# Optimization experiments

Hardware: AMD Instinct MI355X
Metric: run time of the kernel (lower is better)

Reference implementation:

```python
import jax, jax.numpy as jnp
import numpy as np

# ---- module hyperparameters (from init_kwargs) ----
KL_TEMP = 4.0
NUM_CLASSES = 100
POLICY_NUMS = 7          # linear out dim = POLICY_NUMS + 2 (identity, classes, policies)
FEATURE_NUMS = 128       # linear in dim = concat of two 64-d policy features
POS_W = (1.0, 0.5, 0.001)
NEG_W = (1.0, 0.5, 0.001)
KD_CE_W = (1.0, 1.0)
LOSS_W = (1.0, 1.0, 1.0)
BATCH = 2048


def setup_inputs() -> dict:
    key = jax.random.key(0)
    ks = jax.random.split(key, 9)
    O = POLICY_NUMS + 2
    return {
        "student_logits": jax.random.normal(ks[0], (BATCH, NUM_CLASSES), jnp.float32),
        "teacher_logits": jax.random.normal(ks[1], (BATCH, NUM_CLASSES), jnp.float32),
        "student_policy": jax.random.normal(ks[2], (BATCH, FEATURE_NUMS // 2), jnp.float32),
        "teacher_policy": jax.random.normal(ks[3], (BATCH, FEATURE_NUMS // 2), jnp.float32),
        "W1": jax.random.normal(ks[4], (O, FEATURE_NUMS), jnp.float32) * 0.08,  # frozen teacher linear
        "bias1": jax.random.normal(ks[5], (O,), jnp.float32) * 0.01,
        "W2": jax.random.normal(ks[6], (O, FEATURE_NUMS), jnp.float32) * 0.08,  # trainable student linear
        "bias2": jax.random.normal(ks[7], (O,), jnp.float32) * 0.01,
        "targets": jax.random.randint(ks[8], (BATCH, 1, POLICY_NUMS + 1), 0, 10, dtype=jnp.int32),
    }


def _kldiv_mean(inp, tgt):
    # torch KLDivLoss(reduction='mean'): mean over all elems of target*(log(target)-input), zero where target<=0
    safe = jnp.where(tgt > 0, tgt, 1.0)
    return jnp.where(tgt > 0, tgt * (jnp.log(safe) - inp), 0.0).mean()


def _wmean(loss, tgt, pw, nw):
    return jnp.where(tgt == 1.0, loss * pw, loss * nw).mean()


def _pair_linear(feat, W, bias):
    # L[i, j] = W @ concat(f_even[j], f_odd[i]) + bias, computed without materializing [b1,b1,2f]
    f = feat.shape[-1]
    f1, f2 = feat[0::2], feat[1::2]                       # [b1, f] each
    A = f1 @ W[:, :f].T                                   # [b1, O]  (j part)
    B = f2 @ W[:, f:].T                                   # [b1, O]  (i part)
    return B[:, None, :] + A[None, :, :] + bias           # [b1, b1, O]


def _policy_loss(teacher_policy, student_policy, targets, W1, bias1, W2, bias2):
    B = student_policy.shape[0]
    b1 = B // 2
    dt = student_policy.dtype

    Ls = _pair_linear(student_policy, W2, bias2)          # [b1,b1,O]
    Lt = jax.lax.stop_gradient(_pair_linear(teacher_policy, W1, bias1))

    sI, sC = Ls[..., 0], Ls[..., 1]
    sP = Ls[..., 2:].reshape(b1 * b1, POLICY_NUMS)
    tI, tC = Lt[..., 0], Lt[..., 1]
    tP = Lt[..., 2:].reshape(b1 * b1, POLICY_NUMS)

    eye = jnp.eye(b1, dtype=dt)
    # off-diagonal identity entries are detached for the student (teacher already no-grad)
    sI = eye * sI + (1.0 - eye) * jax.lax.stop_gradient(sI)

    t = targets.reshape(B, POLICY_NUMS + 1)
    t1, t2 = t[0::2], t[1::2]
    Teq = (t1[None, :, :] == t2[:, None, :]).astype(dt)   # [b1,b1,P+1]

    classes_value = 1.0 / (NUM_CLASSES - 1) + 1.0
    identity_value = 1.0 / (b1 - 1) + 1.0
    gC = Teq[..., 0] * classes_value - 1.0 / (NUM_CLASSES - 1)
    gP = Teq[..., 1:].reshape(b1 * b1, POLICY_NUMS) * 2.0 - 1.0
    gI = eye * identity_value - 1.0 / (b1 - 1)

    kl_loss = (_wmean((sI - tI) ** 2, gI, POS_W[0], NEG_W[0])
               + _wmean((sC - tC) ** 2, gC, POS_W[1], NEG_W[1])
               + _wmean((sP - tP) ** 2, gP, POS_W[2], NEG_W[2]))

    # KLDivLoss(reduction='mean') returns a scalar; torch.where broadcasts it, so .mean() of weights scales it
    ce_loss = (_kldiv_mean(sI, gI) * jnp.where(gI == 1.0, POS_W[0], NEG_W[0]).mean()
               + _kldiv_mean(sC, gC) * jnp.where(gC == 1.0, POS_W[1], NEG_W[1]).mean()
               + _wmean((sP - gP) ** 2, gP, POS_W[2], NEG_W[2]))

    return KD_CE_W[0] * kl_loss + KD_CE_W[1] * ce_loss


def reference(student_logits, teacher_logits, student_policy, teacher_policy, W1, bias1, W2, bias2, targets):
    B = student_logits.shape[0]
    # ---- CE loss (targets last dim <= 15 -> integer class label at column 0) ----
    labels = targets.reshape(B, -1)[:, 0]
    logp = jax.nn.log_softmax(student_logits, axis=1)
    ce_loss = -jnp.take_along_axis(logp, labels[:, None], axis=1).mean()

    # ---- KD KL loss (KLDivLoss reduction='mean' over all elements) ----
    t_prob = jax.nn.softmax(teacher_logits / KL_TEMP, axis=1)
    s_logp = jax.nn.log_softmax(student_logits / KL_TEMP, axis=1)
    kl_loss = _kldiv_mean(s_logp, t_prob) * (KL_TEMP ** 2)

    # ---- pairwise policy loss (the fusion-heavy path) ----
    policy_loss = _policy_loss(teacher_policy, student_policy, targets, W1, bias1, W2, bias2)

    return LOSS_W[0] * ce_loss + LOSS_W[1] * kl_loss + LOSS_W[2] * policy_loss
```

## Files before the change

kernel.cpp:

```cpp
#include <hip/hip_runtime.h>
#include <math.h>

#define NCLS   100
#define BATCH_ 2048
#define OK     9
#define FHALF  64

#define NLOGB  128
#define NPOLB  16
#define NBLK   (NLOGB + NPOLB)

#define LP_OFF 0
#define PS_OFF (LP_OFF + NLOGB * 2)
#define PB_OFF (PS_OFF + NPOLB * 72)

__device__ __forceinline__ float waveSum(float v) {
#pragma unroll
    for (int off = 32; off; off >>= 1) v += __shfl_xor(v, off, 64);
    return v;
}
__device__ __forceinline__ float waveMax(float v) {
#pragma unroll
    for (int off = 32; off; off >>= 1) v = fmaxf(v, __shfl_xor(v, off, 64));
    return v;
}

__global__ __launch_bounds__(1024) void stats_kernel(
        const float* __restrict__ slog, const float* __restrict__ tlog,
        const float* __restrict__ spol, const float* __restrict__ tpol,
        const float* __restrict__ W1,   const float* __restrict__ W2,
        const int*   __restrict__ tgt,  float* __restrict__ ws)
{
    __shared__ float w1s[OK * 128];
    __shared__ float w2s[OK * 128];
    __shared__ float bkt[320];
    __shared__ float redL[32];

    const int tid  = threadIdx.x;
    const int wave = tid >> 6;
    const int lane = tid & 63;

    if (blockIdx.x < NLOGB) {
        const int r = blockIdx.x * 16 + wave;
        const float* x = slog + r * NCLS;
        const float* y = tlog + r * NCLS;
        const int label = tgt[r * 8];
        const bool has2 = lane < (NCLS - 64);
        float x1 = x[lane];
        float y1 = y[lane];
        float x2 = has2 ? x[lane + 64] : -3.0e38f;
        float y2 = has2 ? y[lane + 64] : -3.0e38f;
        float xl = x[label];
        float mx = waveMax(fmaxf(x1, x2));
        float my = waveMax(fmaxf(y1, y2));
        float se1  = waveSum(expf(x1 - mx) + (has2 ? expf(x2 - mx) : 0.f));
        float se4s = waveSum(expf((x1 - mx) * 0.25f) + (has2 ? expf((x2 - mx) * 0.25f) : 0.f));
        float e1 = expf((y1 - my) * 0.25f);
        float e2 = has2 ? expf((y2 - my) * 0.25f) : 0.f;
        float se4t = waveSum(e1 + e2);
        float tnum = waveSum(e1 * (y1 - x1) * 0.25f + (has2 ? e2 * (y2 - x2) * 0.25f : 0.f));
        if (lane == 0) {
            float logZ1  = mx + logf(se1);
            float logZ4s = mx * 0.25f + logf(se4s);
            float logZ4t = my * 0.25f + logf(se4t);
            redL[wave * 2]     = logZ1 - xl;
            redL[wave * 2 + 1] = tnum / se4t + logZ4s - logZ4t;
        }
        __syncthreads();
        if (tid < 2) {
            float s = 0.f;
#pragma unroll
            for (int w = 0; w < 16; ++w) s += redL[w * 2 + tid];
            ws[LP_OFF + blockIdx.x * 2 + tid] = s;
        }
    } else {
        const int pb = blockIdx.x - NLOGB;
        for (int idx = tid; idx < OK * 128; idx += 1024) { w1s[idx] = W1[idx]; w2s[idx] = W2[idx]; }
        if (tid < 320) bkt[tid] = 0.f;
        __syncthreads();

        float As[OK], Bs[OK];
        if (tid < 64) {
            const int i = pb * 64 + tid;
            const float4* f1s = (const float4*)(spol + (2 * i) * FHALF);
            const float4* f2s = (const float4*)(spol + (2 * i + 1) * FHALF);
            const float4* f1t = (const float4*)(tpol + (2 * i) * FHALF);
            const float4* f2t = (const float4*)(tpol + (2 * i + 1) * FHALF);

            float At[OK], Bt[OK];
#pragma unroll
            for (int k = 0; k < OK; ++k) { As[k] = 0.f; Bs[k] = 0.f; At[k] = 0.f; Bt[k] = 0.f; }
            for (int f4 = 0; f4 < FHALF / 4; ++f4) {
                float4 a4 = f1s[f4], b4 = f2s[f4], c4 = f1t[f4], d4 = f2t[f4];
                const float* ap = (const float*)&a4;
                const float* bp = (const float*)&b4;
                const float* cp = (const float*)&c4;
                const float* dp = (const float*)&d4;
#pragma unroll
                for (int j = 0; j < 4; ++j) {
                    const int f = f4 * 4 + j;
                    const float av = ap[j], bv = bp[j], cv = cp[j], dv = dp[j];
#pragma unroll
                    for (int k = 0; k < OK; ++k) {
                        As[k] = fmaf(av, w2s[k * 128 + f],      As[k]);
                        Bs[k] = fmaf(bv, w2s[k * 128 + 64 + f], Bs[k]);
                        At[k] = fmaf(cv, w1s[k * 128 + f],      At[k]);
                        Bt[k] = fmaf(dv, w1s[k * 128 + 64 + f], Bt[k]);
                    }
                }
            }

#pragma unroll
            for (int k = 0; k < OK; ++k) {
                float du = Bs[k] - Bt[k], dw = As[k] - At[k];
                float v0 = waveSum(du),     v1 = waveSum(du * du);
                float v2 = waveSum(dw),     v3 = waveSum(dw * dw);
                float v4 = waveSum(Bs[k]),  v5 = waveSum(Bs[k] * Bs[k]);
                float v6 = waveSum(As[k]),  v7 = waveSum(As[k] * As[k]);
                if (lane == 0) {
                    float* p = ws + PS_OFF + pb * 72 + k * 8;
                    p[0] = v0; p[1] = v1; p[2] = v2; p[3] = v3;
                    p[4] = v4; p[5] = v5; p[6] = v6; p[7] = v7;
                }
            }

            const int* t1r = tgt + (2 * i) * 8;
            const int* t2r = tgt + (2 * i + 1) * 8;
#pragma unroll
            for (int c0 = 0; c0 < 8; ++c0) {
                int v1i = t1r[c0], v2i = t2r[c0];
                atomicAdd(&bkt[0 * 80 + c0 * 10 + v1i], 1.0f);
                atomicAdd(&bkt[1 * 80 + c0 * 10 + v2i], 1.0f);
                atomicAdd(&bkt[2 * 80 + c0 * 10 + v1i], As[c0 + 1]);
                atomicAdd(&bkt[3 * 80 + c0 * 10 + v2i], Bs[c0 + 1]);
            }
        }
        __syncthreads();
        if (tid < 320) ws[PB_OFF + pb * 320 + tid] = bkt[tid];
    }
}

__global__ __launch_bounds__(256) void combine_kernel(
        const float* __restrict__ ws,
        const float* __restrict__ bias1, const float* __restrict__ bias2,
        float* __restrict__ out)
{
    __shared__ float statsC[72];
    __shared__ float bktC[320];
    __shared__ float cekl[8];

    const int tid  = threadIdx.x;
    const int wave = tid >> 6;
    const int lane = tid & 63;

    float ce = 0.f, kl = 0.f;
    if (tid < NLOGB) {
        ce = ws[LP_OFF + tid * 2];
        kl = ws[LP_OFF + tid * 2 + 1];
    }
    ce = waveSum(ce); kl = waveSum(kl);
    if (lane == 0) { cekl[wave * 2] = ce; cekl[wave * 2 + 1] = kl; }

    if (tid < 72) {
        float s = 0.f;
#pragma unroll
        for (int b = 0; b < NPOLB; ++b) s += ws[PS_OFF + b * 72 + tid];
        statsC[tid] = s;
    }
    for (int idx = tid; idx < 320; idx += 256) {
        float s = 0.f;
#pragma unroll
        for (int b = 0; b < NPOLB; ++b) s += ws[PB_OFF + b * 320 + idx];
        bktC[idx] = s;
    }
    __syncthreads();

    if (tid == 0) {
        const double N = 1024.0, M = 1048576.0;
        double ce_main = (double)(cekl[0] + cekl[2] + cekl[4] + cekl[6]) / (double)BATCH_;
        double kl_main = (double)(cekl[1] + cekl[3] + cekl[5] + cekl[7]) * 16.0
                       / (double)(BATCH_ * NCLS);

        double kl_pol = 0.0, Sp_acc = 0.0;
        double SumL[OK], SumL2[OK];
        for (int k = 0; k < OK; ++k) {
            const float* p = &statsC[k * 8];
            double D1u = p[0], D2u = p[1], D1w = p[2], D2w = p[3];
            double U1 = p[4], U2 = p[5], Wa1 = p[6], Wa2 = p[7];
            double cd = (double)bias2[k] - (double)bias1[k];
            double b  = (double)bias2[k];
            double S = N * D2u + N * (D2w + 2.0 * cd * D1w + N * cd * cd)
                     + 2.0 * D1u * (D1w + N * cd);
            if (k == 0)      kl_pol += S / M;
            else if (k == 1) kl_pol += 0.5 * S / M;
            else             Sp_acc += S;
            SumL[k]  = N * U1 + N * Wa1 + M * b;
            SumL2[k] = N * U2 + N * (Wa2 + 2.0 * b * Wa1 + N * b * b)
                     + 2.0 * U1 * (Wa1 + N * b);
        }
        kl_pol += 0.001 * Sp_acc / (7.0 * M);

        double ce_I = -((double)statsC[4] + (double)statsC[6] + N * (double)bias2[0]) / M;

        const float* cnt1 = &bktC[0];
        const float* cnt2 = &bktC[80];
        const float* sA   = &bktC[160];
        const float* sB   = &bktC[240];
        double ce_C = 0.0, ceP = 0.0;
        for (int c0 = 0; c0 < 8; ++c0) {
            double ms = 0.0, pc = 0.0;
            for (int v = 0; v < 10; ++v) {
                double c1 = (double)cnt1[c0 * 10 + v], c2 = (double)cnt2[c0 * 10 + v];
                ms += c1 * (double)sB[c0 * 10 + v] + c2 * (double)sA[c0 * 10 + v];
                pc += c1 * c2;
            }
            ms += (double)bias2[c0 + 1] * pc;
            if (c0 == 0) {
                ce_C = -0.5 * ms / M;
            } else {
                int k = c0 + 1;
                double sg = 2.0 * ms - SumL[k];
                ceP += SumL2[k] - 2.0 * sg + M;
            }
        }
        ceP *= 0.001 / (7.0 * M);

        out[0] = (float)(ce_main + kl_main + kl_pol + ce_I + ce_C + ceP);
    }
}

extern "C" void kernel_launch(void* const* d_in, const int* in_sizes, int n_in,
                              void* d_out, int out_size, void* d_ws, size_t ws_size,
                              hipStream_t stream) {
    const float* slog = (const float*)d_in[0];
    const float* tlog = (const float*)d_in[1];
    const float* spol = (const float*)d_in[2];
    const float* tpol = (const float*)d_in[3];
    const float* W1   = (const float*)d_in[4];
    const float* b1   = (const float*)d_in[5];
    const float* W2   = (const float*)d_in[6];
    const float* b2   = (const float*)d_in[7];
    const int*   tgt  = (const int*)d_in[8];
    float* ws = (float*)d_ws;

    stats_kernel<<<NBLK, 1024, 0, stream>>>(slog, tlog, spol, tpol, W1, W2, tgt, ws);
    combine_kernel<<<1, 256, 0, stream>>>(ws, b1, b2, (float*)d_out);
}
```

Baseline: 96.71 us.

## Fuse combine into stats kernel via last-block atomic counter; read weights from global

Merges the two kernels into one. Each block bumps a global arrival counter, and the last block to arrive does the final reduction, which removes the second kernel launch and its dependency gap. It also drops the shared-memory staging of W1/W2 and loads the weights as float4 straight from global/cache inside the policy matmul loop. The risks are correctness subtleties in the threadfence/counter protocol and more global load traffic per thread for the weights.

```diff
diff --git a/kernel.cpp b/kernel.cpp
--- a/kernel.cpp
+++ b/kernel.cpp
@@ -14,6 +14,8 @@
 #define PS_OFF (LP_OFF + NLOGB * 2)
 #define PB_OFF (PS_OFF + NPOLB * 72)
 
+__device__ int g_arrive = 0;
+
 __device__ __forceinline__ float waveSum(float v) {
 #pragma unroll
     for (int off = 32; off; off >>= 1) v += __shfl_xor(v, off, 64);
@@ -25,16 +27,20 @@
     return v;
 }
 
-__global__ __launch_bounds__(1024) void stats_kernel(
+__global__ __launch_bounds__(1024) void fused_kernel(
         const float* __restrict__ slog, const float* __restrict__ tlog,
         const float* __restrict__ spol, const float* __restrict__ tpol,
         const float* __restrict__ W1,   const float* __restrict__ W2,
-        const int*   __restrict__ tgt,  float* __restrict__ ws)
+        const int*   __restrict__ tgt,
+        const float* __restrict__ bias1, const float* __restrict__ bias2,
+        float* __restrict__ ws, float* __restrict__ out)
 {
-    __shared__ float w1s[OK * 128];
-    __shared__ float w2s[OK * 128];
     __shared__ float bkt[320];
     __shared__ float redL[32];
+    __shared__ float statsC[72];
+    __shared__ float bktC[320];
+    __shared__ float cekl[8];
+    __shared__ int   lastFlag;
 
     const int tid  = threadIdx.x;
     const int wave = tid >> 6;
@@ -75,7 +81,6 @@
         }
     } else {
         const int pb = blockIdx.x - NLOGB;
-        for (int idx = tid; idx < OK * 128; idx += 1024) { w1s[idx] = W1[idx]; w2s[idx] = W2[idx]; }
         if (tid < 320) bkt[tid] = 0.f;
         __syncthreads();
 
@@ -86,27 +91,36 @@
             const float4* f2s = (const float4*)(spol + (2 * i + 1) * FHALF);
             const float4* f1t = (const float4*)(tpol + (2 * i) * FHALF);
             const float4* f2t = (const float4*)(tpol + (2 * i + 1) * FHALF);
+            const float4* w1q = (const float4*)W1;
+            const float4* w2q = (const float4*)W2;
 
             float At[OK], Bt[OK];
 #pragma unroll
             for (int k = 0; k < OK; ++k) { As[k] = 0.f; Bs[k] = 0.f; At[k] = 0.f; Bt[k] = 0.f; }
             for (int f4 = 0; f4 < FHALF / 4; ++f4) {
                 float4 a4 = f1s[f4], b4 = f2s[f4], c4 = f1t[f4], d4 = f2t[f4];
-                const float* ap = (const float*)&a4;
-                const float* bp = (const float*)&b4;
-                const float* cp = (const float*)&c4;
-                const float* dp = (const float*)&d4;
-#pragma unroll
-                for (int j = 0; j < 4; ++j) {
-                    const int f = f4 * 4 + j;
-                    const float av = ap[j], bv = bp[j], cv = cp[j], dv = dp[j];
-#pragma unroll
-                    for (int k = 0; k < OK; ++k) {
-                        As[k] = fmaf(av, w2s[k * 128 + f],      As[k]);
-                        Bs[k] = fmaf(bv, w2s[k * 128 + 64 + f], Bs[k]);
-                        At[k] = fmaf(cv, w1s[k * 128 + f],      At[k]);
-                        Bt[k] = fmaf(dv, w1s[k * 128 + 64 + f], Bt[k]);
-                    }
+#pragma unroll
+                for (int k = 0; k < OK; ++k) {
+                    const float4 wa2 = w2q[k * 32 + f4];
+                    const float4 wb2 = w2q[k * 32 + 16 + f4];
+                    const float4 wa1 = w1q[k * 32 + f4];
+                    const float4 wb1 = w1q[k * 32 + 16 + f4];
+                    As[k] = fmaf(a4.x, wa2.x, As[k]);
+                    As[k] = fmaf(a4.y, wa2.y, As[k]);
+                    As[k] = fmaf(a4.z, wa2.z, As[k]);
+                    As[k] = fmaf(a4.w, wa2.w, As[k]);
+                    Bs[k] = fmaf(b4.x, wb2.x, Bs[k]);
+                    Bs[k] = fmaf(b4.y, wb2.y, Bs[k]);
+                    Bs[k] = fmaf(b4.z, wb2.z, Bs[k]);
+                    Bs[k] = fmaf(b4.w, wb2.w, Bs[k]);
+                    At[k] = fmaf(c4.x, wa1.x, At[k]);
+                    At[k] = fmaf(c4.y, wa1.y, At[k]);
+                    At[k] = fmaf(c4.z, wa1.z, At[k]);
+                    At[k] = fmaf(c4.w, wa1.w, At[k]);
+                    Bt[k] = fmaf(d4.x, wb1.x, Bt[k]);
+                    Bt[k] = fmaf(d4.y, wb1.y, Bt[k]);
+                    Bt[k] = fmaf(d4.z, wb1.z, Bt[k]);
+                    Bt[k] = fmaf(d4.w, wb1.w, Bt[k]);
                 }
             }
 
@@ -138,20 +152,20 @@
         __syncthreads();
         if (tid < 320) ws[PB_OFF + pb * 320 + tid] = bkt[tid];
     }
-}
-
-__global__ __launch_bounds__(256) void combine_kernel(
-        const float* __restrict__ ws,
-        const float* __restrict__ bias1, const float* __restrict__ bias2,
-        float* __restrict__ out)
-{
-    __shared__ float statsC[72];
-    __shared__ float bktC[320];
-    __shared__ float cekl[8];
-
-    const int tid  = threadIdx.x;
-    const int wave = tid >> 6;
-    const int lane = tid & 63;
+
+    __syncthreads();
+    if (tid == 0) {
+        __threadfence();
+        int old = atomicAdd(&g_arrive, 1);
+        int last = (old == NBLK - 1);
+        if (last) {
+            g_arrive = 0;
+            __threadfence();
+        }
+        lastFlag = last;
+    }
+    __syncthreads();
+    if (!lastFlag) return;
 
     float ce = 0.f, kl = 0.f;
     if (tid < NLOGB) {
@@ -159,7 +173,7 @@
         kl = ws[LP_OFF + tid * 2 + 1];
     }
     ce = waveSum(ce); kl = waveSum(kl);
-    if (lane == 0) { cekl[wave * 2] = ce; cekl[wave * 2 + 1] = kl; }
+    if (lane == 0 && wave < 2) { cekl[wave * 2] = ce; cekl[wave * 2 + 1] = kl; }
 
     if (tid < 72) {
         float s = 0.f;
@@ -167,18 +181,18 @@
         for (int b = 0; b < NPOLB; ++b) s += ws[PS_OFF + b * 72 + tid];
         statsC[tid] = s;
     }
-    for (int idx = tid; idx < 320; idx += 256) {
+    if (tid < 320) {
         float s = 0.f;
 #pragma unroll
-        for (int b = 0; b < NPOLB; ++b) s += ws[PB_OFF + b * 320 + idx];
-        bktC[idx] = s;
+        for (int b = 0; b < NPOLB; ++b) s += ws[PB_OFF + b * 320 + tid];
+        bktC[tid] = s;
     }
     __syncthreads();
 
     if (tid == 0) {
         const double N = 1024.0, M = 1048576.0;
-        double ce_main = (double)(cekl[0] + cekl[2] + cekl[4] + cekl[6]) / (double)BATCH_;
-        double kl_main = (double)(cekl[1] + cekl[3] + cekl[5] + cekl[7]) * 16.0
+        double ce_main = (double)(cekl[0] + cekl[2]) / (double)BATCH_;
+        double kl_main = (double)(cekl[1] + cekl[3]) * 16.0
                        / (double)(BATCH_ * NCLS);
 
         double kl_pol = 0.0, Sp_acc = 0.0;
@@ -243,6 +257,6 @@
     const int*   tgt  = (const int*)d_in[8];
     float* ws = (float*)d_ws;
 
-    stats_kernel<<<NBLK, 1024, 0, stream>>>(slog, tlog, spol, tpol, W1, W2, tgt, ws);
-    combine_kernel<<<1, 256, 0, stream>>>(ws, b1, b2, (float*)d_out);
-}
+    fused_kernel<<<NBLK, 1024, 0, stream>>>(slog, tlog, spol, tpol, W1, W2, tgt,
+                                            b1, b2, ws, (float*)d_out);
+}
```

Result: slower. 107.8 us (+11.5%).
